# Kernel optimization log

Measured on AMD Instinct MI355X. Metric: run time of the kernel, lower is better.

The kernel has to match this reference:

```python
import jax, jax.numpy as jnp
import numpy as np

N = 50000
E = 400000
IN_DIM = 256
H1, D1 = 4, 128   # gat1: heads=4, hidden=128, concat -> 512
H2, D2 = 1, 64    # gat2: heads=1, out=64, concat=False
NEG_SLOPE = 0.2


def setup_inputs() -> dict:
    key = jax.random.key(0)
    ks = jax.random.split(key, 12)
    x = jax.random.normal(ks[0], (N, IN_DIM), dtype=jnp.float32)
    edge_index = jax.random.randint(ks[1], (2, E), 0, N, dtype=jnp.int64)
    edge_attr = jax.random.normal(ks[2], (E,), dtype=jnp.float32)
    # Glorot-ish init for weights, zeros for biases (as in PyG GATConv)
    def glorot(k, shape):
        fan = shape[0] + shape[-1]
        return jax.random.normal(k, shape, dtype=jnp.float32) * jnp.sqrt(2.0 / fan)
    W1 = glorot(ks[3], (IN_DIM, H1 * D1))
    a1_src = glorot(ks[4], (H1, D1))
    a1_dst = glorot(ks[5], (H1, D1))
    b1 = jnp.zeros((H1 * D1,), dtype=jnp.float32)
    W2 = glorot(ks[6], (H1 * D1, H2 * D2))
    a2_src = glorot(ks[7], (H2, D2))
    a2_dst = glorot(ks[8], (H2, D2))
    b2 = jnp.zeros((D2,), dtype=jnp.float32)
    return {"x": x, "edge_index": edge_index, "edge_attr": edge_attr,
            "W1": W1, "a1_src": a1_src, "a1_dst": a1_dst, "b1": b1,
            "W2": W2, "a2_src": a2_src, "a2_dst": a2_dst, "b2": b2}


def _gat_layer(x, src, dst, W, a_s, a_d, b, heads, d, concat):
    n = x.shape[0]
    h = (x @ W).reshape(n, heads, d)                      # [N,H,D]
    alpha_s = jnp.einsum('nhd,hd->nh', h, a_s)            # [N,H]
    alpha_d = jnp.einsum('nhd,hd->nh', h, a_d)
    e = jax.nn.leaky_relu(alpha_s[src] + alpha_d[dst], NEG_SLOPE)  # [Etot,H]
    # segment softmax over incoming edges of each dst node
    emax = jax.ops.segment_max(e, dst, num_segments=n)
    ex = jnp.exp(e - emax[dst])
    denom = jax.ops.segment_sum(ex, dst, num_segments=n)
    alpha = ex / (denom[dst] + 1e-16)                     # [Etot,H]
    msg = h[src] * alpha[:, :, None]                      # [Etot,H,D]
    out = jax.ops.segment_sum(msg, dst, num_segments=n)   # [N,H,D]
    out = out.reshape(n, heads * d) if concat else out.mean(axis=1)
    return out + b


def reference(x, edge_index, edge_attr, W1, a1_src, a1_dst, b1,
              W2, a2_src, a2_dst, b2):
    # edge_attr is ignored (GATConv built without edge_dim)
    loop = jnp.arange(N, dtype=edge_index.dtype)          # PyG add_self_loops=True
    src = jnp.concatenate([edge_index[0], loop])
    dst = jnp.concatenate([edge_index[1], loop])
    h = _gat_layer(x, src, dst, W1, a1_src, a1_dst, b1, H1, D1, True)
    h = jax.nn.elu(h)
    out = _gat_layer(h, src, dst, W2, a2_src, a2_dst, b2, H2, D2, False)
    return out
```

## Files before the change

kernel.cpp:

```cpp
#include <hip/hip_runtime.h>
#include <cstdint>

typedef unsigned short u16;
typedef short bf16x8_t __attribute__((ext_vector_type(8)));
typedef float f32x4_t __attribute__((ext_vector_type(4)));

#define DEVFN __device__ __forceinline__

DEVFN u16 f2bf(float f) {
  unsigned u = __builtin_bit_cast(unsigned, f);
  u = (u + 0x7fffu + ((u >> 16) & 1u)) >> 16;
  return (u16)u;
}
DEVFN float bf2f(u16 s) {
  unsigned u = ((unsigned)s) << 16;
  return __builtin_bit_cast(float, u);
}

DEVFN void gload_lds16(const u16* g, u16* l) {
  __builtin_amdgcn_global_load_lds(
      (const __attribute__((address_space(1))) void*)g,
      (__attribute__((address_space(3))) void*)l, 16, 0, 0);
}

__global__ void prep_kernel(const float* __restrict__ x, const float* __restrict__ W1,
                            const float* __restrict__ W2, const int* __restrict__ edst,
                            u16* __restrict__ xb, u16* __restrict__ w1t, u16* __restrict__ w2t,
                            int* __restrict__ cnt, long nx, int e) {
  const int nxb = (int)((nx + 1023) / 1024);
  int b = blockIdx.x;
  if (b < nxb) {
    long i = ((long)b * 256 + threadIdx.x) * 4;
    if (i + 4 <= nx) {
      float4 v = *reinterpret_cast<const float4*>(x + i);
      uint2 pack;
      pack.x = (unsigned)f2bf(v.x) | ((unsigned)f2bf(v.y) << 16);
      pack.y = (unsigned)f2bf(v.z) | ((unsigned)f2bf(v.w) << 16);
      *reinterpret_cast<uint2*>(xb + i) = pack;
    }
  } else if (b < nxb + 512) {
    int idx = (b - nxb) * 256 + threadIdx.x;
    int k = idx >> 9, m = idx & 511;
    w1t[m * 256 + k] = f2bf(W1[idx]);
  } else if (b < nxb + 512 + 128) {
    int idx = (b - nxb - 512) * 256 + threadIdx.x;
    int k = idx >> 6, m = idx & 63;
    w2t[m * 512 + k] = f2bf(W2[idx]);
  } else {
    int i = (b - nxb - 640) * 256 + threadIdx.x;
    if (i < e) atomicAdd(&cnt[edst[i]], 1);
  }
}

template<int BM, int BN, int WROWS, int K, int BK, int H, int DH>
__global__ __launch_bounds__(256) void gemm_alpha_kernel(
    const u16* __restrict__ A, const u16* __restrict__ BT, u16* __restrict__ C,
    const float* __restrict__ a_s, const float* __restrict__ a_d,
    float* __restrict__ as_out, float* __restrict__ ad_out, int M, int N)
{
  static_assert(BN == DH, "alpha store ownership");
  constexpr int WM = BM / WROWS;
  constexpr int MF = WM / 16;
  constexpr int NF = BN / 16;
  constexpr int KK = BK / 32;
  __shared__ __align__(16) u16 sA[BM][BK];
  __shared__ __align__(16) u16 sB[BN][BK];

  const int tid = threadIdx.x;
  const int lane = tid & 63;
  const int wr = tid >> 6;
  const int brow = blockIdx.x * BM;
  const int bcol = blockIdx.y * BN;

  f32x4_t acc[MF][NF];
#pragma unroll
  for (int i = 0; i < MF; ++i)
#pragma unroll
    for (int j = 0; j < NF; ++j) acc[i][j] = f32x4_t{0.f, 0.f, 0.f, 0.f};

  const int rsel = lane & 15;
  const int kgrp = (lane >> 4) * 8;

#pragma unroll
  for (int k0 = 0; k0 < K; k0 += BK) {
    constexpr int RA = BM * BK / 2048;
#pragma unroll
    for (int c = 0; c < RA; ++c) {
      int t = c * 256 + tid;
      int row = t * 8 / BK;
      int col = (t * 8) % BK;
      int gr = brow + row; gr = gr < M ? gr : M - 1;
      gload_lds16(A + (size_t)gr * K + k0 + col, &sA[0][0] + t * 8);
    }
    constexpr int RB = BN * BK / 2048;
#pragma unroll
    for (int c = 0; c < RB; ++c) {
      int t = c * 256 + tid;
      int row = t * 8 / BK;
      int col = (t * 8) % BK;
      gload_lds16(BT + (size_t)(bcol + row) * K + k0 + col, &sB[0][0] + t * 8);
    }
    __syncthreads();
#pragma unroll
    for (int kk = 0; kk < KK; ++kk) {
      bf16x8_t af[MF], bfr[NF];
#pragma unroll
      for (int i = 0; i < MF; ++i)
        af[i] = *reinterpret_cast<const bf16x8_t*>(&sA[wr * WM + i * 16 + rsel][kk * 32 + kgrp]);
#pragma unroll
      for (int j = 0; j < NF; ++j)
        bfr[j] = *reinterpret_cast<const bf16x8_t*>(&sB[j * 16 + rsel][kk * 32 + kgrp]);
#pragma unroll
      for (int i = 0; i < MF; ++i)
#pragma unroll
        for (int j = 0; j < NF; ++j)
          acc[i][j] = __builtin_amdgcn_mfma_f32_16x16x32_bf16(af[i], bfr[j], acc[i][j], 0, 0, 0);
    }
    __syncthreads();
  }

  const int crow0 = (lane >> 4) * 4;
  const int ccol = lane & 15;

#pragma unroll
  for (int i = 0; i < MF; ++i)
#pragma unroll
    for (int j = 0; j < NF; ++j)
#pragma unroll
      for (int r = 0; r < 4; ++r) {
        int gr = brow + wr * WM + i * 16 + crow0 + r;
        int gc = bcol + j * 16 + ccol;
        if (gr < M) C[(size_t)gr * N + gc] = f2bf(acc[i][j][r]);
      }

  const int head = bcol / DH;
  float asv[NF], adv[NF];
#pragma unroll
  for (int j = 0; j < NF; ++j) {
    int gc = bcol + j * 16 + ccol;
    asv[j] = a_s[gc];
    adv[j] = a_d[gc];
  }
#pragma unroll
  for (int i = 0; i < MF; ++i) {
#pragma unroll
    for (int r = 0; r < 4; ++r) {
      float ps = 0.f, pd = 0.f;
#pragma unroll
      for (int j = 0; j < NF; ++j) {
        float v = acc[i][j][r];
        ps = fmaf(v, asv[j], ps);
        pd = fmaf(v, adv[j], pd);
      }
#pragma unroll
      for (int d = 1; d < 16; d <<= 1) {
        ps += __shfl_xor(ps, d, 64);
        pd += __shfl_xor(pd, d, 64);
      }
      if ((lane & 15) == 0) {
        int gr = brow + wr * WM + i * 16 + crow0 + r;
        if (gr < M) {
          as_out[(size_t)gr * H + head] = ps;
          ad_out[(size_t)gr * H + head] = pd;
        }
      }
    }
  }
}

DEVFN int block_scan_256(int v, int tid, int* wsum) {
#pragma unroll
  for (int d = 1; d < 64; d <<= 1) {
    int u = __shfl_up(v, d, 64);
    if ((tid & 63) >= d) v += u;
  }
  if ((tid & 63) == 63) wsum[tid >> 6] = v;
  __syncthreads();
  int add = 0;
#pragma unroll
  for (int w = 0; w < 4; ++w) add += (w < (tid >> 6)) ? wsum[w] : 0;
  __syncthreads();
  return v + add;
}

__global__ __launch_bounds__(256) void scan_a_kernel(const int* __restrict__ cnt, int* __restrict__ bsum, int n) {
  __shared__ int ws4[4];
  int i = blockIdx.x * 256 + threadIdx.x;
  int v = (i < n) ? cnt[i] + 1 : 0;
  int incl = block_scan_256(v, threadIdx.x, ws4);
  if (threadIdx.x == 255) bsum[blockIdx.x] = incl;
}

__global__ __launch_bounds__(256) void scan_c_kernel(
    const int* __restrict__ cnt, const int* __restrict__ bsum,
    int* __restrict__ rowoff, int* __restrict__ cursor, int n)
{
  __shared__ int ws4[4];
  __shared__ int ws4b[4];
  __shared__ int base_sh;
  int pre = 0;
  for (int w = threadIdx.x; w < blockIdx.x; w += 256) pre += bsum[w];
#pragma unroll
  for (int d = 1; d < 64; d <<= 1) pre += __shfl_xor(pre, d, 64);
  if ((threadIdx.x & 63) == 0) ws4b[threadIdx.x >> 6] = pre;
  __syncthreads();
  if (threadIdx.x == 0) base_sh = ws4b[0] + ws4b[1] + ws4b[2] + ws4b[3];
  int i = blockIdx.x * 256 + threadIdx.x;
  int v = (i < n) ? cnt[i] + 1 : 0;
  int incl = block_scan_256(v, threadIdx.x, ws4);
  int off = base_sh + incl - v;
  if (i < n) {
    rowoff[i] = off;
    cursor[i] = off;
    if (i == n - 1) rowoff[n] = off + v;
  }
}

__global__ void scatter_kernel(const int* __restrict__ srcs, const int* __restrict__ dsts,
                               int* __restrict__ cursor, int* __restrict__ csr, int e, int n) {
  int i = blockIdx.x * 256 + threadIdx.x;
  if (i >= e + n) return;
  int s, d;
  if (i < e) { s = srcs[i]; d = dsts[i]; }
  else       { s = i - e; d = s; }
  int pos = atomicAdd(&cursor[d], 1);
  csr[pos] = s;
}

__global__ __launch_bounds__(256) void agg1_kernel(
    const u16* __restrict__ h1, const float* __restrict__ as1,
    const float* __restrict__ ad1, const int* __restrict__ rowoff,
    const int* __restrict__ csr, const float* __restrict__ b1,
    u16* __restrict__ out, int n)
{
  int node = (blockIdx.x * 256 + threadIdx.x) >> 6;
  int lane = threadIdx.x & 63;
  if (node >= n) return;
  const unsigned head = lane >> 4;
  const unsigned dimbase = lane * 8;
  int e0 = rowoff[node], e1 = rowoff[node + 1];
  float advn = ad1[((unsigned)node << 2) + head];

  float acc[8];
#pragma unroll
  for (int j = 0; j < 8; ++j) acc[j] = 0.f;
  float den = 0.f;

  for (int e = e0; e < e1; ++e) {
    unsigned s = (unsigned)csr[e];
    float t = as1[(s << 2) + head] + advn;
    float l = fmaxf(t, 0.2f * t);
    float ex = __expf(l);
    den += ex;
    bf16x8_t hv = *reinterpret_cast<const bf16x8_t*>(h1 + ((s << 9) + dimbase));
#pragma unroll
    for (int j = 0; j < 8; ++j) acc[j] = fmaf(ex, bf2f((u16)hv[j]), acc[j]);
  }

  float inv = 1.f / (den + 1e-16f);
  u16* orow = out + (((unsigned)node << 9) + dimbase);
#pragma unroll
  for (int j = 0; j < 8; ++j) {
    float v = acc[j] * inv + b1[dimbase + j];
    v = v > 0.f ? v : expm1f(v);
    orow[j] = f2bf(v);
  }
}

__global__ __launch_bounds__(256) void agg2_kernel(
    const u16* __restrict__ h2, const float* __restrict__ as2,
    const float* __restrict__ ad2, const int* __restrict__ rowoff,
    const int* __restrict__ csr, const float* __restrict__ b2,
    float* __restrict__ out, int n)
{
  int node = (blockIdx.x * 256 + threadIdx.x) >> 5;
  int l32 = threadIdx.x & 31;
  if (node >= n) return;
  int e0 = rowoff[node], e1 = rowoff[node + 1];
  float advn = ad2[node];

  float acc0 = 0.f, acc1 = 0.f, den = 0.f;
  for (int e = e0; e < e1; ++e) {
    unsigned s = (unsigned)csr[e];
    float t = as2[s] + advn;
    float l = fmaxf(t, 0.2f * t);
    float ex = __expf(l);
    den += ex;
    unsigned hv = *reinterpret_cast<const unsigned*>(h2 + (s << 6) + l32 * 2);
    acc0 = fmaf(ex, bf2f((u16)(hv & 0xffffu)), acc0);
    acc1 = fmaf(ex, bf2f((u16)(hv >> 16)), acc1);
  }
  float inv = 1.f / (den + 1e-16f);
  float2 o;
  o.x = acc0 * inv + b2[l32 * 2];
  o.y = acc1 * inv + b2[l32 * 2 + 1];
  *reinterpret_cast<float2*>(out + (((size_t)node) << 6) + l32 * 2) = o;
}

extern "C" void kernel_launch(void* const* d_in, const int* in_sizes, int n_in,
                              void* d_out, int out_size, void* d_ws, size_t ws_size,
                              hipStream_t stream) {
  const float* x   = (const float*)d_in[0];
  const int*   ei  = (const int*)d_in[1];
  const float* W1  = (const float*)d_in[3];
  const float* a1s = (const float*)d_in[4];
  const float* a1d = (const float*)d_in[5];
  const float* b1  = (const float*)d_in[6];
  const float* W2  = (const float*)d_in[7];
  const float* a2s = (const float*)d_in[8];
  const float* a2d = (const float*)d_in[9];
  const float* b2  = (const float*)d_in[10];
  float* out = (float*)d_out;

  const int IN_DIM = 256, H1D1 = 512, D2 = 64;
  const int N = in_sizes[0] / IN_DIM;
  const int E = in_sizes[1] / 2;

  char* ws = (char*)d_ws;
  size_t off = 0;
  auto alloc = [&](size_t bytes) -> void* {
    void* p = ws + off;
    off += (bytes + 255) & ~(size_t)255;
    return p;
  };
  u16*  xb     = (u16*)alloc((size_t)N * IN_DIM * 2);
  u16*  w1t    = (u16*)alloc((size_t)H1D1 * IN_DIM * 2);
  u16*  w2t    = (u16*)alloc((size_t)D2 * H1D1 * 2);
  u16*  h1b    = (u16*)alloc((size_t)N * H1D1 * 2);
  int*  cnt    = (int*)alloc((size_t)N * 4);
  float* as1   = (float*)alloc((size_t)N * 4 * 4);
  float* ad1   = (float*)alloc((size_t)N * 4 * 4);
  float* as2   = (float*)alloc((size_t)N * 4);
  float* ad2   = (float*)alloc((size_t)N * 4);
  int*  cursor = (int*)alloc((size_t)N * 4);
  int*  rowoff = (int*)alloc((size_t)(N + 1) * 4);
  int*  bsum   = (int*)alloc(256 * 4);
  int*  csr    = (int*)alloc((size_t)(E + N) * 4);
  u16*  h1o    = (u16*)alloc((size_t)N * H1D1 * 2);
  u16*  h2b    = (u16*)alloc((size_t)N * D2 * 2);
  (void)n_in; (void)out_size; (void)ws_size;

  const int* esrc = ei;
  const int* edst = ei + E;

  hipMemsetAsync(cnt, 0, (size_t)N * 4, stream);

  long nx = (long)N * IN_DIM;
  int nxb = (int)((nx + 1023) / 1024);
  int eb = (E + 255) / 256;
  prep_kernel<<<nxb + 640 + eb, 256, 0, stream>>>(x, W1, W2, edst, xb, w1t, w2t, cnt, nx, E);

  dim3 g1((N + 127) / 128, H1D1 / 128);
  gemm_alpha_kernel<128, 128, 4, 256, 64, 4, 128><<<g1, 256, 0, stream>>>(
      xb, w1t, h1b, a1s, a1d, as1, ad1, N, H1D1);

  int nsb = (N + 255) / 256;
  scan_a_kernel<<<nsb, 256, 0, stream>>>(cnt, bsum, N);
  scan_c_kernel<<<nsb, 256, 0, stream>>>(cnt, bsum, rowoff, cursor, N);
  scatter_kernel<<<(E + N + 255) / 256, 256, 0, stream>>>(esrc, edst, cursor, csr, E, N);

  agg1_kernel<<<(N + 3) / 4, 256, 0, stream>>>(h1b, as1, ad1, rowoff, csr, b1, h1o, N);

  dim3 g2((N + 63) / 64, 1);
  gemm_alpha_kernel<64, 64, 4, 512, 64, 1, 64><<<g2, 256, 0, stream>>>(
      h1o, w2t, h2b, a2s, a2d, as2, ad2, N, D2);

  agg2_kernel<<<((size_t)N * 32 + 255) / 256, 256, 0, stream>>>(h2b, as2, ad2, rowoff, csr, b2, out, N);
}
```

Measured before the change: 253.8 us.

## Fuse x fp32-to-bf16 conversion into layer-1 GEMM and remap blocks per XCD

The separate pass that converted x to a bf16 buffer is removed. The first GEMM now reads fp32 x directly, converts it in registers and writes it into LDS, which saves one full write and re-read of the 50000x256 activation. The launch also becomes a 1D grid where the four column tiles of the same row block share an XCD (bid&7), so repeated A reads can hit the same L2. The trade-off is that the A tile is now loaded synchronously through VGPRs instead of with global_load_lds, and each of the four column blocks re-converts the same fp32 rows.

Measured after the change: 245.7 us. 3.2% less time.

```diff
diff --git a/kernel.cpp b/kernel.cpp
--- a/kernel.cpp
+++ b/kernel.cpp
@@ -16,6 +16,9 @@
   unsigned u = ((unsigned)s) << 16;
   return __builtin_bit_cast(float, u);
 }
+DEVFN unsigned pk2bf(float a, float b) {
+  return (unsigned)f2bf(a) | ((unsigned)f2bf(b) << 16);
+}
 
 DEVFN void gload_lds16(const u16* g, u16* l) {
   __builtin_amdgcn_global_load_lds(
@@ -23,32 +26,155 @@
       (__attribute__((address_space(3))) void*)l, 16, 0, 0);
 }
 
-__global__ void prep_kernel(const float* __restrict__ x, const float* __restrict__ W1,
-                            const float* __restrict__ W2, const int* __restrict__ edst,
-                            u16* __restrict__ xb, u16* __restrict__ w1t, u16* __restrict__ w2t,
-                            int* __restrict__ cnt, long nx, int e) {
-  const int nxb = (int)((nx + 1023) / 1024);
+__global__ void prep_kernel(const float* __restrict__ W1, const float* __restrict__ W2,
+                            const int* __restrict__ edst,
+                            u16* __restrict__ w1t, u16* __restrict__ w2t,
+                            int* __restrict__ cnt, int e) {
   int b = blockIdx.x;
-  if (b < nxb) {
-    long i = ((long)b * 256 + threadIdx.x) * 4;
-    if (i + 4 <= nx) {
-      float4 v = *reinterpret_cast<const float4*>(x + i);
-      uint2 pack;
-      pack.x = (unsigned)f2bf(v.x) | ((unsigned)f2bf(v.y) << 16);
-      pack.y = (unsigned)f2bf(v.z) | ((unsigned)f2bf(v.w) << 16);
-      *reinterpret_cast<uint2*>(xb + i) = pack;
-    }
-  } else if (b < nxb + 512) {
-    int idx = (b - nxb) * 256 + threadIdx.x;
+  if (b < 512) {
+    int idx = b * 256 + threadIdx.x;
     int k = idx >> 9, m = idx & 511;
     w1t[m * 256 + k] = f2bf(W1[idx]);
-  } else if (b < nxb + 512 + 128) {
-    int idx = (b - nxb - 512) * 256 + threadIdx.x;
+  } else if (b < 512 + 128) {
+    int idx = (b - 512) * 256 + threadIdx.x;
     int k = idx >> 6, m = idx & 63;
     w2t[m * 512 + k] = f2bf(W2[idx]);
   } else {
-    int i = (b - nxb - 640) * 256 + threadIdx.x;
+    int i = (b - 640) * 256 + threadIdx.x;
     if (i < e) atomicAdd(&cnt[edst[i]], 1);
+  }
+}
+
+template<int BM, int BN, int WROWS, int K, int BK, int NP, int H, int DH>
+__global__ __launch_bounds__(256) void gemm1_alpha_kernel(
+    const float* __restrict__ A, const u16* __restrict__ BT, u16* __restrict__ C,
+    const float* __restrict__ a_s, const float* __restrict__ a_d,
+    float* __restrict__ as_out, float* __restrict__ ad_out, int M)
+{
+  constexpr int N = NP * BN;
+  constexpr int WM = BM / WROWS;
+  constexpr int MF = WM / 16;
+  constexpr int NF = BN / 16;
+  constexpr int KK = BK / 32;
+  __shared__ __align__(16) u16 sA[BM][BK];
+  __shared__ __align__(16) u16 sB[BN][BK];
+
+  const int tid = threadIdx.x;
+  const int lane = tid & 63;
+  const int wr = tid >> 6;
+
+  const int bid = blockIdx.x;
+  const int xcd = bid & 7;
+  const int rest = bid >> 3;
+  const int p = rest & (NP - 1);
+  const int rb = rest / NP;
+  const int r = rb * 8 + xcd;
+  const int NRB = (M + BM - 1) / BM;
+  if (r >= NRB) return;
+  const int brow = r * BM;
+  const int bcol = p * BN;
+
+  f32x4_t acc[MF][NF];
+#pragma unroll
+  for (int i = 0; i < MF; ++i)
+#pragma unroll
+    for (int j = 0; j < NF; ++j) acc[i][j] = f32x4_t{0.f, 0.f, 0.f, 0.f};
+
+  const int rsel = lane & 15;
+  const int kgrp = (lane >> 4) * 8;
+
+#pragma unroll
+  for (int k0 = 0; k0 < K; k0 += BK) {
+    constexpr int RA = BM * BK / 2048;
+#pragma unroll
+    for (int c = 0; c < RA; ++c) {
+      int q = c * 256 + tid;
+      int row = q * 8 / BK;
+      int col8 = (q * 8) % BK;
+      int gr = brow + row; gr = gr < M ? gr : M - 1;
+      const float* src = A + (size_t)gr * K + k0 + col8;
+      float4 v0 = *reinterpret_cast<const float4*>(src);
+      float4 v1 = *reinterpret_cast<const float4*>(src + 4);
+      uint4 pk;
+      pk.x = pk2bf(v0.x, v0.y);
+      pk.y = pk2bf(v0.z, v0.w);
+      pk.z = pk2bf(v1.x, v1.y);
+      pk.w = pk2bf(v1.z, v1.w);
+      *reinterpret_cast<uint4*>(&sA[row][col8]) = pk;
+    }
+    constexpr int RB = BN * BK / 2048;
+#pragma unroll
+    for (int c = 0; c < RB; ++c) {
+      int t = c * 256 + tid;
+      int row = t * 8 / BK;
+      int col = (t * 8) % BK;
+      gload_lds16(BT + (size_t)(bcol + row) * K + k0 + col, &sB[0][0] + t * 8);
+    }
+    __syncthreads();
+#pragma unroll
+    for (int kk = 0; kk < KK; ++kk) {
+      bf16x8_t af[MF], bfr[NF];
+#pragma unroll
+      for (int i = 0; i < MF; ++i)
+        af[i] = *reinterpret_cast<const bf16x8_t*>(&sA[wr * WM + i * 16 + rsel][kk * 32 + kgrp]);
+#pragma unroll
+      for (int j = 0; j < NF; ++j)
+        bfr[j] = *reinterpret_cast<const bf16x8_t*>(&sB[j * 16 + rsel][kk * 32 + kgrp]);
+#pragma unroll
+      for (int i = 0; i < MF; ++i)
+#pragma unroll
+        for (int j = 0; j < NF; ++j)
+          acc[i][j] = __builtin_amdgcn_mfma_f32_16x16x32_bf16(af[i], bfr[j], acc[i][j], 0, 0, 0);
+    }
+    __syncthreads();
+  }
+
+  const int crow0 = (lane >> 4) * 4;
+  const int ccol = lane & 15;
+
+#pragma unroll
+  for (int i = 0; i < MF; ++i)
+#pragma unroll
+    for (int j = 0; j < NF; ++j)
+#pragma unroll
+      for (int rr = 0; rr < 4; ++rr) {
+        int gr = brow + wr * WM + i * 16 + crow0 + rr;
+        int gc = bcol + j * 16 + ccol;
+        if (gr < M) C[(size_t)gr * N + gc] = f2bf(acc[i][j][rr]);
+      }
+
+  const int head = bcol / DH;
+  float asv[NF], adv[NF];
+#pragma unroll
+  for (int j = 0; j < NF; ++j) {
+    int gc = bcol + j * 16 + ccol;
+    asv[j] = a_s[gc];
+    adv[j] = a_d[gc];
+  }
+#pragma unroll
+  for (int i = 0; i < MF; ++i) {
+#pragma unroll
+    for (int rr = 0; rr < 4; ++rr) {
+      float ps = 0.f, pd = 0.f;
+#pragma unroll
+      for (int j = 0; j < NF; ++j) {
+        float v = acc[i][j][rr];
+        ps = fmaf(v, asv[j], ps);
+        pd = fmaf(v, adv[j], pd);
+      }
+#pragma unroll
+      for (int d = 1; d < 16; d <<= 1) {
+        ps += __shfl_xor(ps, d, 64);
+        pd += __shfl_xor(pd, d, 64);
+      }
+      if ((lane & 15) == 0) {
+        int gr = brow + wr * WM + i * 16 + crow0 + rr;
+        if (gr < M) {
+          as_out[(size_t)gr * H + head] = ps;
+          ad_out[(size_t)gr * H + head] = pd;
+        }
+      }
+    }
   }
 }
 
@@ -127,10 +253,10 @@
 #pragma unroll
     for (int j = 0; j < NF; ++j)
 #pragma unroll
-      for (int r = 0; r < 4; ++r) {
-        int gr = brow + wr * WM + i * 16 + crow0 + r;
+      for (int rr = 0; rr < 4; ++rr) {
+        int gr = brow + wr * WM + i * 16 + crow0 + rr;
         int gc = bcol + j * 16 + ccol;
-        if (gr < M) C[(size_t)gr * N + gc] = f2bf(acc[i][j][r]);
+        if (gr < M) C[(size_t)gr * N + gc] = f2bf(acc[i][j][rr]);
       }
 
   const int head = bcol / DH;
@@ -144,11 +270,11 @@
 #pragma unroll
   for (int i = 0; i < MF; ++i) {
 #pragma unroll
-    for (int r = 0; r < 4; ++r) {
+    for (int rr = 0; rr < 4; ++rr) {
       float ps = 0.f, pd = 0.f;
 #pragma unroll
       for (int j = 0; j < NF; ++j) {
-        float v = acc[i][j][r];
+        float v = acc[i][j][rr];
         ps = fmaf(v, asv[j], ps);
         pd = fmaf(v, adv[j], pd);
       }
@@ -158,7 +284,7 @@
         pd += __shfl_xor(pd, d, 64);
       }
       if ((lane & 15) == 0) {
-        int gr = brow + wr * WM + i * 16 + crow0 + r;
+        int gr = brow + wr * WM + i * 16 + crow0 + rr;
         if (gr < M) {
           as_out[(size_t)gr * H + head] = ps;
           ad_out[(size_t)gr * H + head] = pd;
@@ -323,7 +449,6 @@
     off += (bytes + 255) & ~(size_t)255;
     return p;
   };
-  u16*  xb     = (u16*)alloc((size_t)N * IN_DIM * 2);
   u16*  w1t    = (u16*)alloc((size_t)H1D1 * IN_DIM * 2);
   u16*  w2t    = (u16*)alloc((size_t)D2 * H1D1 * 2);
   u16*  h1b    = (u16*)alloc((size_t)N * H1D1 * 2);
@@ -343,16 +468,15 @@
   const int* esrc = ei;
   const int* edst = ei + E;
 
-  hipMemsetAsync(cnt, 0, (size_t)N * 4, stream);
-
-  long nx = (long)N * IN_DIM;
-  int nxb = (int)((nx + 1023) / 1024);
+  (void)hipMemsetAsync(cnt, 0, (size_t)N * 4, stream);
+
   int eb = (E + 255) / 256;
-  prep_kernel<<<nxb + 640 + eb, 256, 0, stream>>>(x, W1, W2, edst, xb, w1t, w2t, cnt, nx, E);
-
-  dim3 g1((N + 127) / 128, H1D1 / 128);
-  gemm_alpha_kernel<128, 128, 4, 256, 64, 4, 128><<<g1, 256, 0, stream>>>(
-      xb, w1t, h1b, a1s, a1d, as1, ad1, N, H1D1);
+  prep_kernel<<<640 + eb, 256, 0, stream>>>(W1, W2, edst, w1t, w2t, cnt, E);
+
+  const int NRB = (N + 127) / 128;
+  const int g1 = ((NRB + 7) / 8) * 8 * 4;
+  gemm1_alpha_kernel<128, 128, 4, 256, 64, 4, 4, 128><<<g1, 256, 0, stream>>>(
+      x, w1t, h1b, a1s, a1d, as1, ad1, N);
 
   int nsb = (N + 255) / 256;
   scan_a_kernel<<<nsb, 256, 0, stream>>>(cnt, bsum, N);
```
